# Kernel optimization log

Hardware: AMD Instinct MI355X
Metric: run time of the kernel (lower is better)

The kernel has to match this reference:

```python
import jax, jax.numpy as jnp
import numpy as np

N_NODES = 100000
N_EDGES = 1600000


def setup_inputs() -> dict:
    key = jax.random.key(0)
    ks = jax.random.split(key, 6)
    x = jax.random.normal(ks[0], (N_NODES, 166), dtype=jnp.float32)
    edge_index = jax.random.randint(ks[1], (2, N_EDGES), 0, N_NODES, dtype=jnp.int64)
    s = 0.05
    return {
        "x": x,
        "edge_index": edge_index,
        "W1l": jax.random.normal(ks[2], (166, 128), dtype=jnp.float32) * s,
        "b1": jnp.zeros((128,), dtype=jnp.float32),
        "W1r": jax.random.normal(ks[3], (166, 128), dtype=jnp.float32) * s,
        "W2l": jax.random.normal(ks[4], (128, 2), dtype=jnp.float32) * s,
        "b2": jnp.zeros((2,), dtype=jnp.float32),
        "W2r": jax.random.normal(ks[5], (128, 2), dtype=jnp.float32) * s,
    }


def _sage_mean_agg(h, src, dst, n_nodes):
    # mean over incoming edges (PyG SAGEConv default aggr='mean');
    # nodes with no in-edges get zeros.
    summed = jax.ops.segment_sum(h[src], dst, num_segments=n_nodes)
    deg = jax.ops.segment_sum(jnp.ones_like(dst, dtype=h.dtype), dst,
                              num_segments=n_nodes)
    return summed / jnp.maximum(deg, 1.0)[:, None]


def reference(x, edge_index, W1l, b1, W1r, W2l, b2, W2r):
    src, dst = edge_index[0], edge_index[1]
    n = x.shape[0]
    # layer 1: out = lin_l(mean_agg(x)) + lin_r(x)
    agg1 = _sage_mean_agg(x, src, dst, n)
    h = agg1 @ W1l + b1 + x @ W1r
    h = jax.nn.relu(h)
    # dropout p=0.5 is identity in eval mode
    # layer 2
    agg2 = _sage_mean_agg(h, src, dst, n)
    out = agg2 @ W2l + b2 + h @ W2r
    return jax.nn.log_softmax(out, axis=1)
```

## Files before the change

kernel.cpp:

```cpp
#include <hip/hip_runtime.h>
#include <hip/hip_bf16.h>
#include <math.h>

#define N_NODES 100000
#define N_EDGES 1600000
#define FDIM 166
#define HDIM 128
#define KP 192
#define CAP 48
#define YTP 264
#define MBLK 64
#define XCHUNKS 43
#define XPITCH 688
#define TOTCH (MBLK * XCHUNKS)
#define NXCD 8
#define NODES_PER (N_NODES / NXCD)

typedef __attribute__((ext_vector_type(8))) short bf16x8;
typedef __attribute__((ext_vector_type(4))) float f32x4;

#define GLOAD_LDS16(g, l) __builtin_amdgcn_global_load_lds( \
    (const __attribute__((address_space(1))) unsigned int*)(g), \
    (__attribute__((address_space(3))) unsigned int*)(l), 16, 0, 0)

__device__ inline float bf2f(unsigned short s) {
    unsigned int u = ((unsigned int)s) << 16;
    float f; __builtin_memcpy(&f, &u, 4); return f;
}
__device__ inline float bflo(unsigned int u) {
    unsigned int v = u << 16;
    float f; __builtin_memcpy(&f, &v, 4); return f;
}
__device__ inline float bfhi(unsigned int u) {
    unsigned int v = u & 0xffff0000u;
    float f; __builtin_memcpy(&f, &v, 4); return f;
}
__device__ inline unsigned short f2bf(float f) {
    unsigned int u; __builtin_memcpy(&u, &f, 4);
    unsigned int r = u + 0x7fffu + ((u >> 16) & 1u);
    return (unsigned short)(r >> 16);
}
__device__ inline bf16x8 pack8(float4 a, float4 b) {
    union { bf16x8 v; __hip_bfloat162 h[4]; } u;
    u.h[0] = __float22bfloat162_rn(make_float2(a.x, a.y));
    u.h[1] = __float22bfloat162_rn(make_float2(a.z, a.w));
    u.h[2] = __float22bfloat162_rn(make_float2(b.x, b.y));
    u.h[3] = __float22bfloat162_rn(make_float2(b.z, b.w));
    return u.v;
}

__global__ void k_pre(const float* __restrict__ W1l, const float* __restrict__ W1r,
                      unsigned short* __restrict__ wt, int* __restrict__ cnt) {
    int idx = blockIdx.x * 256 + threadIdx.x;
    if (blockIdx.x < 192) {
        int c = idx / KP, k = idx - c * KP;
        float v = 0.f;
        if (k < FDIM)
            v = (c < HDIM) ? W1l[k * HDIM + c] : W1r[k * HDIM + (c - HDIM)];
        wt[idx] = f2bf(v);
    } else {
        int i = idx - 192 * 256;
        if (i < N_NODES) cnt[i] = 0;
    }
}

__global__ __launch_bounds__(256) void k_fill(const int* __restrict__ ei,
                                              int* __restrict__ cnt,
                                              int* __restrict__ adj) {
    int xcd = blockIdx.x & (NXCD - 1);
    int grp = blockIdx.x >> 3;
    int lo = xcd * NODES_PER, hi = lo + NODES_PER;
    int stride = (gridDim.x >> 3) * 256;
    for (int e = grp * 256 + threadIdx.x; e < N_EDGES; e += stride) {
        int d = ei[N_EDGES + e];
        int s = ei[e];
        if (d >= lo && d < hi) {
            int slot = atomicAdd(&cnt[d], 1);
            if (slot < CAP) adj[d * CAP + slot] = s;
        }
    }
}

__global__ __launch_bounds__(256) void k_gemm(
        const float* __restrict__ x, const unsigned short* __restrict__ wt,
        unsigned short* __restrict__ yl, unsigned short* __restrict__ yr) {
    __shared__ __align__(16) char sm[44160];
    int tid = threadIdx.x;
    int r0 = blockIdx.x * MBLK;
    int w = tid >> 6, lane = tid & 63;

    if (tid < 32) *(float*)(sm + TOTCH * 16 + tid * 4) = 0.f;

    {
        int wbase = w * 64;
        #pragma unroll
        for (int rd = 0; rd < 11; ++rd) {
            int base = rd * 256 + wbase;
            if (base < TOTCH) {
                int idx = base + lane;
                int row = idx / XCHUNKS, c = idx - row * XCHUNKS;
                int gr = r0 + row; if (gr > N_NODES - 1) gr = N_NODES - 1;
                int cb = (c == 42) ? 0 : c * 16;
                const char* src = (const char*)x + (size_t)gr * (FDIM * 4) + cb;
                GLOAD_LDS16(src, sm + base * 16);
            }
        }
    }
    __syncthreads();

    int rbase = (w >> 1) * 32;
    int c0 = (w & 1) * 128;
    int l15 = lane & 15, g = lane >> 4;

    f32x4 acc[2][8];
    #pragma unroll
    for (int a = 0; a < 2; a++)
        #pragma unroll
        for (int b = 0; b < 8; b++) acc[a][b] = (f32x4){0.f, 0.f, 0.f, 0.f};

    const char* wb = (const char*)wt;
    int wlane = (c0 + l15) * (KP * 2) + 16 * g;
    int brow0 = (rbase + l15) * XPITCH + 32 * g;
    int brow1 = brow0 + 16 * XPITCH;

    bf16x8 ww[2][8];
    #pragma unroll
    for (int cf = 0; cf < 8; cf++)
        ww[0][cf] = *(const bf16x8*)(wb + wlane + cf * (16 * KP * 2));

    #pragma unroll
    for (int kk = 0; kk < 6; ++kk) {
        int cur = kk & 1, nxt = cur ^ 1;
        if (kk < 5) {
            #pragma unroll
            for (int cf = 0; cf < 8; cf++)
                ww[nxt][cf] = *(const bf16x8*)(wb + wlane + cf * (16 * KP * 2) + (kk + 1) * 64);
        }
        float4 p0 = *(const float4*)(sm + brow0 + kk * 128);
        float4 q0 = *(const float4*)(sm + brow0 + kk * 128 + 16);
        float4 p1 = *(const float4*)(sm + brow1 + kk * 128);
        float4 q1 = *(const float4*)(sm + brow1 + kk * 128 + 16);
        bf16x8 xb0 = pack8(p0, q0);
        bf16x8 xb1 = pack8(p1, q1);
        #pragma unroll
        for (int cf = 0; cf < 8; cf++) {
            acc[0][cf] = __builtin_amdgcn_mfma_f32_16x16x32_bf16(ww[cur][cf], xb0, acc[0][cf], 0, 0, 0);
            acc[1][cf] = __builtin_amdgcn_mfma_f32_16x16x32_bf16(ww[cur][cf], xb1, acc[1][cf], 0, 0, 0);
        }
    }
    __syncthreads();

    #pragma unroll
    for (int rf = 0; rf < 2; rf++) {
        int row = rbase + 16 * rf + l15;
        #pragma unroll
        for (int cf = 0; cf < 8; cf++) {
            int col = c0 + 16 * cf + 4 * g;
            ushort4 o;
            o.x = f2bf(acc[rf][cf][0]); o.y = f2bf(acc[rf][cf][1]);
            o.z = f2bf(acc[rf][cf][2]); o.w = f2bf(acc[rf][cf][3]);
            *(ushort4*)(sm + row * (YTP * 2) + col * 2) = o;
        }
    }
    __syncthreads();

    for (int it = 0; it < 8; ++it) {
        int n = tid + it * 256;
        int row = n >> 5, c16 = n & 31;
        uint4 v = *(const uint4*)(sm + row * (YTP * 2) + c16 * 16);
        int gr = r0 + row;
        if (gr < N_NODES) {
            unsigned short* dst = (c16 < 16) ? yl : yr;
            *(uint4*)((char*)dst + (size_t)gr * 256 + (size_t)(c16 & 15) * 16) = v;
        }
    }
}

__global__ __launch_bounds__(256) void k_agg1(
        const unsigned short* __restrict__ yl, const unsigned short* __restrict__ yr,
        const int* __restrict__ cnt, const int* __restrict__ adj,
        const float* __restrict__ b1,
        const float* __restrict__ W2l, const float* __restrict__ W2r,
        float* __restrict__ zw) {
    int w = threadIdx.x >> 6, lane = threadIdx.x & 63;
    int i = blockIdx.x * 4 + w;
    if (i >= N_NODES) return;
    int deg = cnt[i];
    int n = min(deg, CAP);
    int aidx = adj[i * CAP + lane];
    float a0 = 0.f, a1 = 0.f, p0 = 0.f, p1 = 0.f, q0 = 0.f, q1 = 0.f, r0 = 0.f, r1 = 0.f;
    int j = 0;
    for (; j + 4 <= n; j += 4) {
        int s0 = __shfl(aidx, j, 64);
        int s1 = __shfl(aidx, j + 1, 64);
        int s2 = __shfl(aidx, j + 2, 64);
        int s3 = __shfl(aidx, j + 3, 64);
        unsigned int u0 = *(const unsigned int*)&yl[(size_t)s0 * HDIM + lane * 2];
        unsigned int u1 = *(const unsigned int*)&yl[(size_t)s1 * HDIM + lane * 2];
        unsigned int u2 = *(const unsigned int*)&yl[(size_t)s2 * HDIM + lane * 2];
        unsigned int u3 = *(const unsigned int*)&yl[(size_t)s3 * HDIM + lane * 2];
        a0 += bflo(u0); a1 += bfhi(u0);
        p0 += bflo(u1); p1 += bfhi(u1);
        q0 += bflo(u2); q1 += bfhi(u2);
        r0 += bflo(u3); r1 += bfhi(u3);
    }
    for (; j < n; ++j) {
        int s = __shfl(aidx, j, 64);
        unsigned int u = *(const unsigned int*)&yl[(size_t)s * HDIM + lane * 2];
        a0 += bflo(u); a1 += bfhi(u);
    }
    a0 += p0 + q0 + r0;
    a1 += p1 + q1 + r1;
    float inv = 1.f / (float)max(deg, 1);
    unsigned int ur = *(const unsigned int*)&yr[(size_t)i * HDIM + lane * 2];
    float2 bb = *(const float2*)&b1[lane * 2];
    float h0 = fmaxf(a0 * inv + bflo(ur) + bb.x, 0.f);
    float h1 = fmaxf(a1 * inv + bfhi(ur) + bb.y, 0.f);
    float4 wl2 = *(const float4*)&W2l[lane * 4];
    float4 wr2 = *(const float4*)&W2r[lane * 4];
    float z0 = h0 * wl2.x + h1 * wl2.z;
    float z1 = h0 * wl2.y + h1 * wl2.w;
    float w0 = h0 * wr2.x + h1 * wr2.z;
    float w1 = h0 * wr2.y + h1 * wr2.w;
    #pragma unroll
    for (int m = 32; m; m >>= 1) {
        z0 += __shfl_xor(z0, m, 64); z1 += __shfl_xor(z1, m, 64);
        w0 += __shfl_xor(w0, m, 64); w1 += __shfl_xor(w1, m, 64);
    }
    if (lane == 0) {
        float4 o = {z0, z1, w0, w1};
        *(float4*)&zw[i * 4] = o;
    }
}

__global__ void k_out(const float* __restrict__ zw, const int* __restrict__ cnt,
                      const int* __restrict__ adj, const float* __restrict__ b2,
                      float* __restrict__ out) {
    int i = blockIdx.x * 256 + threadIdx.x;
    if (i >= N_NODES) return;
    int deg = cnt[i];
    int n = min(deg, CAP);
    float s0 = 0.f, s1 = 0.f;
    const int* arow = adj + i * CAP;
    for (int j = 0; j < n; j++) {
        int s = arow[j];
        float2 zz = *(const float2*)&zw[s * 4];
        s0 += zz.x; s1 += zz.y;
    }
    float inv = 1.f / (float)max(deg, 1);
    float p0 = s0 * inv + b2[0] + zw[i * 4 + 2];
    float p1 = s1 * inv + b2[1] + zw[i * 4 + 3];
    float mx = fmaxf(p0, p1);
    float lse = mx + logf(expf(p0 - mx) + expf(p1 - mx));
    out[i * 2 + 0] = p0 - lse;
    out[i * 2 + 1] = p1 - lse;
}

extern "C" void kernel_launch(void* const* d_in, const int* in_sizes, int n_in,
                              void* d_out, int out_size, void* d_ws, size_t ws_size,
                              hipStream_t stream) {
    const float* x   = (const float*)d_in[0];
    const int*   ei  = (const int*)d_in[1];
    const float* W1l = (const float*)d_in[2];
    const float* b1  = (const float*)d_in[3];
    const float* W1r = (const float*)d_in[4];
    const float* W2l = (const float*)d_in[5];
    const float* b2  = (const float*)d_in[6];
    const float* W2r = (const float*)d_in[7];
    float* out = (float*)d_out;

    char* ws = (char*)d_ws;
    size_t off = 0;
    auto alloc = [&](size_t bytes) {
        off = (off + 255) & ~(size_t)255;
        void* p = ws + off;
        off += bytes;
        return p;
    };
    int* cnt            = (int*)alloc((size_t)N_NODES * 4);
    int* adj            = (int*)alloc((size_t)N_NODES * CAP * 4);
    unsigned short* wt  = (unsigned short*)alloc((size_t)256 * KP * 2);
    unsigned short* yl  = (unsigned short*)alloc((size_t)N_NODES * HDIM * 2);
    unsigned short* yr  = (unsigned short*)alloc((size_t)N_NODES * HDIM * 2);
    float* zw           = (float*)alloc((size_t)N_NODES * 4 * 4);
    (void)ws_size; (void)in_sizes; (void)n_in; (void)out_size;

    k_pre<<<192 + (N_NODES + 255) / 256, 256, 0, stream>>>(W1l, W1r, wt, cnt);
    k_fill<<<2048, 256, 0, stream>>>(ei, cnt, adj);
    k_gemm<<<(N_NODES + MBLK - 1) / MBLK, 256, 0, stream>>>(x, wt, yl, yr);
    k_agg1<<<(N_NODES + 3) / 4, 256, 0, stream>>>(yl, yr, cnt, adj, b1, W2l, W2r, zw);
    k_out<<<(N_NODES + 255) / 256, 256, 0, stream>>>(zw, cnt, adj, b2, out);
}
```

Measured before the change: 218.3 us.

## Drop LDS staging in GEMM; load x directly, pre-swizzle weights per lane

The GEMM kernel no longer stages x tiles in LDS through global_load_lds and no longer stages output through LDS. Each lane now reads its x rows straight from global memory and writes bf16 results straight to yl/yr. Weights are pre-swizzled in k_pre into an MFMA-fragment order, so every lane's weight load is one contiguous 16-byte read, and a launch bound of 3 blocks is added. This removes the LDS usage and the barriers to raise occupancy, in exchange for uncoalesced strided global reads of x and narrower 8-byte output stores.

```diff
diff --git a/kernel.cpp b/kernel.cpp
--- a/kernel.cpp
+++ b/kernel.cpp
@@ -8,20 +8,12 @@
 #define HDIM 128
 #define KP 192
 #define CAP 48
-#define YTP 264
 #define MBLK 64
-#define XCHUNKS 43
-#define XPITCH 688
-#define TOTCH (MBLK * XCHUNKS)
 #define NXCD 8
 #define NODES_PER (N_NODES / NXCD)
 
 typedef __attribute__((ext_vector_type(8))) short bf16x8;
 typedef __attribute__((ext_vector_type(4))) float f32x4;
-
-#define GLOAD_LDS16(g, l) __builtin_amdgcn_global_load_lds( \
-    (const __attribute__((address_space(1))) unsigned int*)(g), \
-    (__attribute__((address_space(3))) unsigned int*)(l), 16, 0, 0)
 
 __device__ inline float bf2f(unsigned short s) {
     unsigned int u = ((unsigned int)s) << 16;
@@ -50,14 +42,19 @@
 }
 
 __global__ void k_pre(const float* __restrict__ W1l, const float* __restrict__ W1r,
-                      unsigned short* __restrict__ wt, int* __restrict__ cnt) {
+                      unsigned short* __restrict__ wt2, int* __restrict__ cnt) {
     int idx = blockIdx.x * 256 + threadIdx.x;
     if (blockIdx.x < 192) {
-        int c = idx / KP, k = idx - c * KP;
+        int fb = idx >> 9, r = idx & 511;
+        int lane = r >> 3, j = r & 7;
+        int g = lane >> 4, l15 = lane & 15;
+        int kk = fb / 16, cb = fb & 15;
+        int c = cb * 16 + l15;
+        int k = kk * 32 + 8 * g + j;
         float v = 0.f;
         if (k < FDIM)
             v = (c < HDIM) ? W1l[k * HDIM + c] : W1r[k * HDIM + (c - HDIM)];
-        wt[idx] = f2bf(v);
+        wt2[idx] = f2bf(v);
     } else {
         int i = idx - 192 * 256;
         if (i < N_NODES) cnt[i] = 0;
@@ -81,36 +78,21 @@
     }
 }
 
-__global__ __launch_bounds__(256) void k_gemm(
-        const float* __restrict__ x, const unsigned short* __restrict__ wt,
+__global__ __launch_bounds__(256, 3) void k_gemm(
+        const float* __restrict__ x, const unsigned short* __restrict__ wt2,
         unsigned short* __restrict__ yl, unsigned short* __restrict__ yr) {
-    __shared__ __align__(16) char sm[44160];
     int tid = threadIdx.x;
     int r0 = blockIdx.x * MBLK;
     int w = tid >> 6, lane = tid & 63;
 
-    if (tid < 32) *(float*)(sm + TOTCH * 16 + tid * 4) = 0.f;
-
-    {
-        int wbase = w * 64;
-        #pragma unroll
-        for (int rd = 0; rd < 11; ++rd) {
-            int base = rd * 256 + wbase;
-            if (base < TOTCH) {
-                int idx = base + lane;
-                int row = idx / XCHUNKS, c = idx - row * XCHUNKS;
-                int gr = r0 + row; if (gr > N_NODES - 1) gr = N_NODES - 1;
-                int cb = (c == 42) ? 0 : c * 16;
-                const char* src = (const char*)x + (size_t)gr * (FDIM * 4) + cb;
-                GLOAD_LDS16(src, sm + base * 16);
-            }
-        }
-    }
-    __syncthreads();
-
     int rbase = (w >> 1) * 32;
-    int c0 = (w & 1) * 128;
+    int half = w & 1;
     int l15 = lane & 15, g = lane >> 4;
+
+    int gr0 = r0 + rbase + l15;       if (gr0 > N_NODES - 1) gr0 = N_NODES - 1;
+    int gr1 = gr0 + 16;               if (gr1 > N_NODES - 1) gr1 = N_NODES - 1;
+    const char* xr0 = (const char*)x + (size_t)gr0 * (FDIM * 4) + 32 * g;
+    const char* xr1 = (const char*)x + (size_t)gr1 * (FDIM * 4) + 32 * g;
 
     f32x4 acc[2][8];
     #pragma unroll
@@ -118,60 +100,53 @@
         #pragma unroll
         for (int b = 0; b < 8; b++) acc[a][b] = (f32x4){0.f, 0.f, 0.f, 0.f};
 
-    const char* wb = (const char*)wt;
-    int wlane = (c0 + l15) * (KP * 2) + 16 * g;
-    int brow0 = (rbase + l15) * XPITCH + 32 * g;
-    int brow1 = brow0 + 16 * XPITCH;
-
-    bf16x8 ww[2][8];
-    #pragma unroll
-    for (int cf = 0; cf < 8; cf++)
-        ww[0][cf] = *(const bf16x8*)(wb + wlane + cf * (16 * KP * 2));
-
-    #pragma unroll
+    const char* wb = (const char*)wt2 + (size_t)lane * 16;
+
     for (int kk = 0; kk < 6; ++kk) {
-        int cur = kk & 1, nxt = cur ^ 1;
+        bf16x8 ww[8];
+        #pragma unroll
+        for (int cf = 0; cf < 8; cf++)
+            ww[cf] = *(const bf16x8*)(wb + (size_t)(kk * 16 + half * 8 + cf) * 1024);
+        float4 p0, q0, p1, q1;
         if (kk < 5) {
-            #pragma unroll
-            for (int cf = 0; cf < 8; cf++)
-                ww[nxt][cf] = *(const bf16x8*)(wb + wlane + cf * (16 * KP * 2) + (kk + 1) * 64);
-        }
-        float4 p0 = *(const float4*)(sm + brow0 + kk * 128);
-        float4 q0 = *(const float4*)(sm + brow0 + kk * 128 + 16);
-        float4 p1 = *(const float4*)(sm + brow1 + kk * 128);
-        float4 q1 = *(const float4*)(sm + brow1 + kk * 128 + 16);
+            p0 = *(const float4*)(xr0 + kk * 128);
+            q0 = *(const float4*)(xr0 + kk * 128 + 16);
+            p1 = *(const float4*)(xr1 + kk * 128);
+            q1 = *(const float4*)(xr1 + kk * 128 + 16);
+        } else {
+            if (g == 0) {
+                p0 = *(const float4*)(xr0 + 640);
+                p1 = *(const float4*)(xr1 + 640);
+                float2 t0 = *(const float2*)(xr0 + 656);
+                float2 t1 = *(const float2*)(xr1 + 656);
+                q0 = make_float4(t0.x, t0.y, 0.f, 0.f);
+                q1 = make_float4(t1.x, t1.y, 0.f, 0.f);
+            } else {
+                p0 = make_float4(0.f, 0.f, 0.f, 0.f);
+                q0 = p0; p1 = p0; q1 = p0;
+            }
+        }
         bf16x8 xb0 = pack8(p0, q0);
         bf16x8 xb1 = pack8(p1, q1);
         #pragma unroll
         for (int cf = 0; cf < 8; cf++) {
-            acc[0][cf] = __builtin_amdgcn_mfma_f32_16x16x32_bf16(ww[cur][cf], xb0, acc[0][cf], 0, 0, 0);
-            acc[1][cf] = __builtin_amdgcn_mfma_f32_16x16x32_bf16(ww[cur][cf], xb1, acc[1][cf], 0, 0, 0);
-        }
-    }
-    __syncthreads();
-
+            acc[0][cf] = __builtin_amdgcn_mfma_f32_16x16x32_bf16(ww[cf], xb0, acc[0][cf], 0, 0, 0);
+            acc[1][cf] = __builtin_amdgcn_mfma_f32_16x16x32_bf16(ww[cf], xb1, acc[1][cf], 0, 0, 0);
+        }
+    }
+
+    unsigned short* dst = half ? yr : yl;
     #pragma unroll
     for (int rf = 0; rf < 2; rf++) {
-        int row = rbase + 16 * rf + l15;
-        #pragma unroll
-        for (int cf = 0; cf < 8; cf++) {
-            int col = c0 + 16 * cf + 4 * g;
-            ushort4 o;
-            o.x = f2bf(acc[rf][cf][0]); o.y = f2bf(acc[rf][cf][1]);
-            o.z = f2bf(acc[rf][cf][2]); o.w = f2bf(acc[rf][cf][3]);
-            *(ushort4*)(sm + row * (YTP * 2) + col * 2) = o;
-        }
-    }
-    __syncthreads();
-
-    for (int it = 0; it < 8; ++it) {
-        int n = tid + it * 256;
-        int row = n >> 5, c16 = n & 31;
-        uint4 v = *(const uint4*)(sm + row * (YTP * 2) + c16 * 16);
-        int gr = r0 + row;
+        int gr = r0 + rbase + 16 * rf + l15;
         if (gr < N_NODES) {
-            unsigned short* dst = (c16 < 16) ? yl : yr;
-            *(uint4*)((char*)dst + (size_t)gr * 256 + (size_t)(c16 & 15) * 16) = v;
+            #pragma unroll
+            for (int cf = 0; cf < 8; cf++) {
+                ushort4 o;
+                o.x = f2bf(acc[rf][cf][0]); o.y = f2bf(acc[rf][cf][1]);
+                o.z = f2bf(acc[rf][cf][2]); o.w = f2bf(acc[rf][cf][3]);
+                *(ushort4*)&dst[(size_t)gr * HDIM + 16 * cf + 4 * g] = o;
+            }
         }
     }
 }
@@ -279,15 +254,15 @@
     };
     int* cnt            = (int*)alloc((size_t)N_NODES * 4);
     int* adj            = (int*)alloc((size_t)N_NODES * CAP * 4);
-    unsigned short* wt  = (unsigned short*)alloc((size_t)256 * KP * 2);
+    unsigned short* wt2 = (unsigned short*)alloc((size_t)256 * KP * 2);
     unsigned short* yl  = (unsigned short*)alloc((size_t)N_NODES * HDIM * 2);
     unsigned short* yr  = (unsigned short*)alloc((size_t)N_NODES * HDIM * 2);
     float* zw           = (float*)alloc((size_t)N_NODES * 4 * 4);
     (void)ws_size; (void)in_sizes; (void)n_in; (void)out_size;
 
-    k_pre<<<192 + (N_NODES + 255) / 256, 256, 0, stream>>>(W1l, W1r, wt, cnt);
+    k_pre<<<192 + (N_NODES + 255) / 256, 256, 0, stream>>>(W1l, W1r, wt2, cnt);
     k_fill<<<2048, 256, 0, stream>>>(ei, cnt, adj);
-    k_gemm<<<(N_NODES + MBLK - 1) / MBLK, 256, 0, stream>>>(x, wt, yl, yr);
+    k_gemm<<<(N_NODES + MBLK - 1) / MBLK, 256, 0, stream>>>(x, wt2, yl, yr);
     k_agg1<<<(N_NODES + 3) / 4, 256, 0, stream>>>(yl, yr, cnt, adj, b1, W2l, W2r, zw);
     k_out<<<(N_NODES + 255) / 256, 256, 0, stream>>>(zw, cnt, adj, b2, out);
 }
```

Measured after the change: 202.0 us. 7.5% less time.
